# Kernel tuning notes

Measured on AMD Instinct MI355X. Metric: run time of the kernel, lower is better.

The kernel has to match this reference:

```python
import jax, jax.numpy as jnp
import numpy as np

PATCH = 16
EMBED = 384
BINS = 32
LN_EPS = 1e-5


def setup_inputs() -> dict:
    key = jax.random.key(0)
    k1, k2 = jax.random.split(key, 2)
    images = jax.random.uniform(k1, (64, 3, 224, 224), dtype=jnp.float32)  # pixels in [0,1]
    proj_w = jax.random.normal(k2, (EMBED, 3, PATCH, PATCH), dtype=jnp.float32) * 0.02  # OIHW
    proj_b = jnp.zeros((EMBED,), jnp.float32)
    ln_gamma = jnp.ones((EMBED,), jnp.float32)
    ln_beta = jnp.zeros((EMBED,), jnp.float32)
    return {"images": images, "proj_w": proj_w, "proj_b": proj_b,
            "ln_gamma": ln_gamma, "ln_beta": ln_beta}


def _patch_entropy(images, patch_size):
    # images: (B, C, H, W) in [0,1]
    B, C, H, W = images.shape
    gH, gW = H // patch_size, W // patch_size
    gray = images.mean(axis=1)  # (B, H, W)
    # non-overlapping patches -> (B, N, P*P)
    patches = gray.reshape(B, gH, patch_size, gW, patch_size)
    patches = patches.transpose(0, 1, 3, 2, 4).reshape(B, gH * gW, patch_size * patch_size)
    # quantize to 32 bins (floor, matching torch .long() on non-negative values)
    q = jnp.clip(patches * (BINS - 1), 0, BINS - 1).astype(jnp.int32)
    one_hot = jax.nn.one_hot(q, BINS, dtype=jnp.float32)      # (B, N, P*P, 32)
    hist = one_hot.sum(axis=2)                                 # (B, N, 32)
    prob = hist / jnp.maximum(hist.sum(axis=-1, keepdims=True), 1e-8)
    log_prob = jnp.log2(prob + 1e-10)
    entropy = -(prob * log_prob).sum(axis=-1)                  # (B, N)
    return entropy / np.float32(np.log2(BINS))


def reference(images, proj_w, proj_b, ln_gamma, ln_beta):
    p = PATCH
    B, C, H, W = images.shape
    gH, gW = H // p, W // p
    entropy = _patch_entropy(images, p)
    # patch-embed conv: kernel=stride=patch_size, VALID padding
    x = jax.lax.conv_general_dilated(
        images, proj_w, window_strides=(p, p), padding='VALID',
        dimension_numbers=('NCHW', 'OIHW', 'NCHW'))            # (B, D, gH, gW)
    x = x + proj_b[None, :, None, None]
    x = x.transpose(0, 2, 3, 1).reshape(B, gH * gW, -1)        # (B, N, D)
    mu = x.mean(axis=-1, keepdims=True)
    var = x.var(axis=-1, keepdims=True)                        # biased, like torch LayerNorm
    x = (x - mu) / jnp.sqrt(var + LN_EPS) * ln_gamma + ln_beta
    return x, entropy
```

## Files before the change

### kernel.cpp

```cpp
#include <hip/hip_runtime.h>

#define BATCH 64
#define GH 14
#define GW 14
#define NPATCH (GH*GW)
#define M_ROWS (BATCH*NPATCH)
#define KDIM 768
#define DDIM 384
#define HW (224*224)

typedef __attribute__((ext_vector_type(8))) short s16x8;
typedef __attribute__((ext_vector_type(4))) float f32x4;
typedef __attribute__((ext_vector_type(4))) unsigned short u16x4;

__device__ __forceinline__ unsigned short f2bf(float f) {
    unsigned int u = __float_as_uint(f);
    u += 0x7fff + ((u >> 16) & 1);
    return (unsigned short)(u >> 16);
}

__device__ __forceinline__ s16x8 cvt8(float4 lo, float4 hi) {
    s16x8 o;
    o[0] = (short)f2bf(lo.x); o[1] = (short)f2bf(lo.y);
    o[2] = (short)f2bf(lo.z); o[3] = (short)f2bf(lo.w);
    o[4] = (short)f2bf(hi.x); o[5] = (short)f2bf(hi.y);
    o[6] = (short)f2bf(hi.z); o[7] = (short)f2bf(hi.w);
    return o;
}

__global__ __launch_bounds__(256) void wcast_kernel(const float* __restrict__ w,
                                                    unsigned short* __restrict__ W) {
    int t = blockIdx.x * 256 + threadIdx.x;
    float4 v = ((const float4*)w)[t];
    u16x4 o = { f2bf(v.x), f2bf(v.y), f2bf(v.z), f2bf(v.w) };
    *(u16x4*)(W + t * 4) = o;
}

__global__ __launch_bounds__(384) void fused_kernel(const float* __restrict__ img,
                                                    const unsigned short* __restrict__ Bt,
                                                    const float* __restrict__ bias,
                                                    const float* __restrict__ gamma,
                                                    const float* __restrict__ beta,
                                                    float* __restrict__ C,
                                                    float* __restrict__ ent) {
    __shared__ __align__(16) unsigned short As[32 * 64];
    __shared__ __align__(16) unsigned short Bs[384 * 64];
    __shared__ int hist[6][32];
    __shared__ float sred[32], sred2[32], smean[32], srstd[32];

    const int tid  = threadIdx.x;
    const int lane = tid & 63;
    const int wv   = tid >> 6;
    const int quad = lane >> 4;
    const int cl   = lane & 15;
    const int rowBase = blockIdx.x * 32;

    if (tid < 32) { sred[tid] = 0.0f; sred2[tid] = 0.0f; }

    const int r1  = tid >> 3, ksg = tid & 7;
    const int sA1 = r1 * 64 + (ksg ^ (r1 & 7)) * 8;
    const float* pA1;
    {
        int p = rowBase + r1, b = p / NPATCH, n = p - b * NPATCH;
        int ph = n / GW, pw_ = n - ph * GW;
        pA1 = img + (size_t)b * (3 * HW) + (ph * 16 + (ksg >> 1)) * 224 + pw_ * 16 + (ksg & 1) * 8;
    }
    const unsigned short* pB0 = Bt + (size_t)(tid >> 3) * KDIM + (tid & 7) * 8;
    const int sB = (tid >> 3) * 64 + ((tid & 7) ^ ((tid >> 3) & 7)) * 8;

    s16x8 breg[8];
#pragma unroll
    for (int i = 0; i < 8; ++i)
        breg[i] = *(const s16x8*)(pB0 + (size_t)i * (48 * KDIM));
    float4 a1lo, a1hi;
    if (tid < 256) {
        a1lo = *(const float4*)(pA1);
        a1hi = *(const float4*)(pA1 + 4);
    }

    {
        const int pr  = lane >> 2;
        const int cc4 = (lane & 3) * 4;
        int p0 = rowBase + wv, b0 = p0 / NPATCH, n0i = p0 - b0 * NPATCH;
        int ph0 = n0i / GW, pw0 = n0i - ph0 * GW;
        const float* bp = img + (size_t)b0 * (3 * HW) + (ph0 * 16 + pr) * 224 + pw0 * 16 + cc4;
        float4 c0 = *(const float4*)(bp);
        float4 c1 = *(const float4*)(bp + HW);
        float4 c2 = *(const float4*)(bp + 2 * HW);
        for (int pp = wv; pp < 32; pp += 6) {
            float4 n0, n1, n2;
            if (pp + 6 < 32) {
                int p = rowBase + pp + 6, b = p / NPATCH, n = p - b * NPATCH;
                int ph = n / GW, pw_ = n - ph * GW;
                const float* np = img + (size_t)b * (3 * HW) + (ph * 16 + pr) * 224 + pw_ * 16 + cc4;
                n0 = *(const float4*)(np);
                n1 = *(const float4*)(np + HW);
                n2 = *(const float4*)(np + 2 * HW);
            }
            if (lane < 32) hist[wv][lane] = 0;
            asm volatile("s_waitcnt lgkmcnt(0)" ::: "memory");
            float g[4] = { (c0.x + c1.x + c2.x) / 3.0f, (c0.y + c1.y + c2.y) / 3.0f,
                           (c0.z + c1.z + c2.z) / 3.0f, (c0.w + c1.w + c2.w) / 3.0f };
#pragma unroll
            for (int j = 0; j < 4; ++j) {
                int bin = (int)(g[j] * 31.0f);
                bin = bin < 0 ? 0 : (bin > 31 ? 31 : bin);
                atomicAdd(&hist[wv][bin], 1);
            }
            asm volatile("s_waitcnt lgkmcnt(0)" ::: "memory");
            float t = 0.0f;
            if (lane < 32) {
                float prb = (float)hist[wv][lane] * (1.0f / 256.0f);
                t = -prb * log2f(prb + 1e-10f);
            }
#pragma unroll
            for (int off = 32; off; off >>= 1) t += __shfl_xor(t, off);
            if (lane == 0) ent[rowBase + pp] = t * (1.0f / 5.0f);
            c0 = n0; c1 = n1; c2 = n2;
        }
    }

    if (tid < 256) *(s16x8*)(As + sA1) = cvt8(a1lo, a1hi);
#pragma unroll
    for (int i = 0; i < 8; ++i)
        *(s16x8*)(Bs + sB + i * (48 * 64)) = breg[i];
    __syncthreads();

    f32x4 acc[2][4] = {};
    for (int kt = 0; kt < 12; ++kt) {
        if (kt < 11) {
            const int kn = kt + 1;
            if (tid < 256) {
                const float* pa = pA1 + (kn >> 2) * HW + (kn & 3) * (4 * 224);
                a1lo = *(const float4*)(pa);
                a1hi = *(const float4*)(pa + 4);
            }
#pragma unroll
            for (int i = 0; i < 8; ++i)
                breg[i] = *(const s16x8*)(pB0 + (size_t)i * (48 * KDIM) + kn * 64);
        }
#pragma unroll
        for (int ks = 0; ks < 2; ++ks) {
            const int sw = (ks * 4 + quad) ^ (cl & 7);
            s16x8 a_frag[2], b_frag[4];
#pragma unroll
            for (int i = 0; i < 2; ++i)
                a_frag[i] = *(const s16x8*)(As + (i * 16 + cl) * 64 + sw * 8);
#pragma unroll
            for (int j = 0; j < 4; ++j)
                b_frag[j] = *(const s16x8*)(Bs + (wv * 64 + j * 16 + cl) * 64 + sw * 8);
#pragma unroll
            for (int i = 0; i < 2; ++i)
#pragma unroll
                for (int j = 0; j < 4; ++j)
                    acc[i][j] = __builtin_amdgcn_mfma_f32_16x16x32_bf16(
                        a_frag[i], b_frag[j], acc[i][j], 0, 0, 0);
        }
        __syncthreads();
        if (kt < 11) {
            if (tid < 256) *(s16x8*)(As + sA1) = cvt8(a1lo, a1hi);
#pragma unroll
            for (int i = 0; i < 8; ++i)
                *(s16x8*)(Bs + sB + i * (48 * 64)) = breg[i];
        }
        __syncthreads();
    }

    float bv[4], gv[4], btv[4];
#pragma unroll
    for (int j = 0; j < 4; ++j) {
        int col = wv * 64 + j * 16 + cl;
        bv[j] = bias[col]; gv[j] = gamma[col]; btv[j] = beta[col];
    }

#pragma unroll
    for (int i = 0; i < 2; ++i) {
#pragma unroll
        for (int r = 0; r < 4; ++r) {
            float s1 = 0.0f, s2 = 0.0f;
#pragma unroll
            for (int j = 0; j < 4; ++j) {
                float v = acc[i][j][r] + bv[j];
                s1 += v; s2 += v * v;
            }
#pragma unroll
            for (int off = 1; off < 16; off <<= 1) {
                s1 += __shfl_xor(s1, off);
                s2 += __shfl_xor(s2, off);
            }
            if (cl == 0) {
                int row = i * 16 + quad * 4 + r;
                atomicAdd(&sred[row], s1);
                atomicAdd(&sred2[row], s2);
            }
        }
    }
    __syncthreads();
    if (tid < 32) {
        float mu  = sred[tid] * (1.0f / (float)DDIM);
        float var = sred2[tid] * (1.0f / (float)DDIM) - mu * mu;
        smean[tid] = mu;
        srstd[tid] = rsqrtf(var + 1e-5f);
    }
    __syncthreads();

#pragma unroll
    for (int i = 0; i < 2; ++i) {
#pragma unroll
        for (int r = 0; r < 4; ++r) {
            int row = i * 16 + quad * 4 + r;
            float mu = smean[row], rs = srstd[row];
            float* crow = C + (size_t)(rowBase + row) * DDIM;
#pragma unroll
            for (int j = 0; j < 4; ++j)
                crow[wv * 64 + j * 16 + cl] = (acc[i][j][r] + bv[j] - mu) * rs * gv[j] + btv[j];
        }
    }
}

extern "C" void kernel_launch(void* const* d_in, const int* in_sizes, int n_in,
                              void* d_out, int out_size, void* d_ws, size_t ws_size,
                              hipStream_t stream) {
    const float* img = (const float*)d_in[0];
    const float* pw  = (const float*)d_in[1];
    const float* pb  = (const float*)d_in[2];
    const float* gam = (const float*)d_in[3];
    const float* bet = (const float*)d_in[4];
    float* out = (float*)d_out;

    unsigned short* Wbf = (unsigned short*)d_ws;
    float* ent = out + (size_t)M_ROWS * DDIM;

    hipLaunchKernelGGL(wcast_kernel, dim3(288), dim3(256), 0, stream, pw, Wbf);
    hipLaunchKernelGGL(fused_kernel, dim3(392), dim3(384), 0, stream,
                       img, Wbf, pb, gam, bet, out, ent);
}
```

Baseline: 113.7 us.

## Load weight fragments directly into registers and double-buffer A tiles in LDS

Removes the shared-memory staging of the weight matrix: each wave now loads its MFMA B fragments straight from global memory into registers, with even/odd k-tile register sets prefetched one step ahead. The A tile is double-buffered across two LDS buffers with a register prefetch pipeline, which removes one barrier per k-step. LDS use drops sharply, and launch bounds request 3 blocks per CU for higher occupancy. The cost is more VGPR pressure and uncoalesced, redundant global reads of the weights across blocks, which now rely on the L2 cache.

```diff
diff --git a/kernel.cpp b/kernel.cpp
--- a/kernel.cpp
+++ b/kernel.cpp
@@ -36,15 +36,15 @@
     *(u16x4*)(W + t * 4) = o;
 }
 
-__global__ __launch_bounds__(384) void fused_kernel(const float* __restrict__ img,
-                                                    const unsigned short* __restrict__ Bt,
-                                                    const float* __restrict__ bias,
-                                                    const float* __restrict__ gamma,
-                                                    const float* __restrict__ beta,
-                                                    float* __restrict__ C,
-                                                    float* __restrict__ ent) {
-    __shared__ __align__(16) unsigned short As[32 * 64];
-    __shared__ __align__(16) unsigned short Bs[384 * 64];
+__global__ __launch_bounds__(384, 3) void fused_kernel(const float* __restrict__ img,
+                                                       const unsigned short* __restrict__ Bt,
+                                                       const float* __restrict__ bias,
+                                                       const float* __restrict__ gamma,
+                                                       const float* __restrict__ beta,
+                                                       float* __restrict__ C,
+                                                       float* __restrict__ ent) {
+    __shared__ __align__(16) unsigned short As0[32 * 64];
+    __shared__ __align__(16) unsigned short As1[32 * 64];
     __shared__ int hist[6][32];
     __shared__ float sred[32], sred2[32], smean[32], srstd[32];
 
@@ -65,17 +65,26 @@
         int ph = n / GW, pw_ = n - ph * GW;
         pA1 = img + (size_t)b * (3 * HW) + (ph * 16 + (ksg >> 1)) * 224 + pw_ * 16 + (ksg & 1) * 8;
     }
-    const unsigned short* pB0 = Bt + (size_t)(tid >> 3) * KDIM + (tid & 7) * 8;
-    const int sB = (tid >> 3) * 64 + ((tid & 7) ^ ((tid >> 3) & 7)) * 8;
-
-    s16x8 breg[8];
-#pragma unroll
-    for (int i = 0; i < 8; ++i)
-        breg[i] = *(const s16x8*)(pB0 + (size_t)i * (48 * KDIM));
-    float4 a1lo, a1hi;
+    const unsigned short* pBr = Bt + (size_t)(wv * 64 + cl) * KDIM + quad * 8;
+
+    s16x8 bE[8], bO[8];
+#pragma unroll
+    for (int j = 0; j < 4; ++j)
+#pragma unroll
+        for (int ks = 0; ks < 2; ++ks) {
+            bE[ks * 4 + j] = *(const s16x8*)(pBr + j * (16 * KDIM) + 0 * 64 + ks * 32);
+            bO[ks * 4 + j] = *(const s16x8*)(pBr + j * (16 * KDIM) + 1 * 64 + ks * 32);
+        }
+    float4 a0lo, a0hi, aOlo, aOhi, aElo, aEhi;
     if (tid < 256) {
-        a1lo = *(const float4*)(pA1);
-        a1hi = *(const float4*)(pA1 + 4);
+        a0lo = *(const float4*)(pA1);
+        a0hi = *(const float4*)(pA1 + 4);
+        const float* p1 = pA1 + 1 * (4 * 224);
+        aOlo = *(const float4*)(p1);
+        aOhi = *(const float4*)(p1 + 4);
+        const float* p2 = pA1 + 2 * (4 * 224);
+        aElo = *(const float4*)(p2);
+        aEhi = *(const float4*)(p2 + 4);
     }
 
     {
@@ -120,50 +129,65 @@
         }
     }
 
-    if (tid < 256) *(s16x8*)(As + sA1) = cvt8(a1lo, a1hi);
-#pragma unroll
-    for (int i = 0; i < 8; ++i)
-        *(s16x8*)(Bs + sB + i * (48 * 64)) = breg[i];
+    if (tid < 256) *(s16x8*)(As0 + sA1) = cvt8(a0lo, a0hi);
     __syncthreads();
 
     f32x4 acc[2][4] = {};
-    for (int kt = 0; kt < 12; ++kt) {
-        if (kt < 11) {
-            const int kn = kt + 1;
-            if (tid < 256) {
-                const float* pa = pA1 + (kn >> 2) * HW + (kn & 3) * (4 * 224);
-                a1lo = *(const float4*)(pa);
-                a1hi = *(const float4*)(pa + 4);
-            }
-#pragma unroll
-            for (int i = 0; i < 8; ++i)
-                breg[i] = *(const s16x8*)(pB0 + (size_t)i * (48 * KDIM) + kn * 64);
+#pragma unroll
+    for (int h = 0; h < 6; ++h) {
+        const int t0 = 2 * h;
+        if (tid < 256) *(s16x8*)(As1 + sA1) = cvt8(aOlo, aOhi);
+        if (h < 5 && tid < 256) {
+            const int kn = t0 + 3;
+            const float* p = pA1 + (kn >> 2) * HW + (kn & 3) * (4 * 224);
+            aOlo = *(const float4*)(p);
+            aOhi = *(const float4*)(p + 4);
         }
 #pragma unroll
         for (int ks = 0; ks < 2; ++ks) {
             const int sw = (ks * 4 + quad) ^ (cl & 7);
-            s16x8 a_frag[2], b_frag[4];
-#pragma unroll
-            for (int i = 0; i < 2; ++i)
-                a_frag[i] = *(const s16x8*)(As + (i * 16 + cl) * 64 + sw * 8);
+            s16x8 af0 = *(const s16x8*)(As0 + (0 * 16 + cl) * 64 + sw * 8);
+            s16x8 af1 = *(const s16x8*)(As0 + (1 * 16 + cl) * 64 + sw * 8);
+#pragma unroll
+            for (int j = 0; j < 4; ++j) {
+                acc[0][j] = __builtin_amdgcn_mfma_f32_16x16x32_bf16(af0, bE[ks * 4 + j], acc[0][j], 0, 0, 0);
+                acc[1][j] = __builtin_amdgcn_mfma_f32_16x16x32_bf16(af1, bE[ks * 4 + j], acc[1][j], 0, 0, 0);
+            }
+        }
+        if (h < 5) {
 #pragma unroll
             for (int j = 0; j < 4; ++j)
-                b_frag[j] = *(const s16x8*)(Bs + (wv * 64 + j * 16 + cl) * 64 + sw * 8);
-#pragma unroll
-            for (int i = 0; i < 2; ++i)
-#pragma unroll
-                for (int j = 0; j < 4; ++j)
-                    acc[i][j] = __builtin_amdgcn_mfma_f32_16x16x32_bf16(
-                        a_frag[i], b_frag[j], acc[i][j], 0, 0, 0);
+#pragma unroll
+                for (int ks = 0; ks < 2; ++ks)
+                    bE[ks * 4 + j] = *(const s16x8*)(pBr + j * (16 * KDIM) + (t0 + 2) * 64 + ks * 32);
         }
         __syncthreads();
-        if (kt < 11) {
-            if (tid < 256) *(s16x8*)(As + sA1) = cvt8(a1lo, a1hi);
-#pragma unroll
-            for (int i = 0; i < 8; ++i)
-                *(s16x8*)(Bs + sB + i * (48 * 64)) = breg[i];
-        }
-        __syncthreads();
+        if (h < 5 && tid < 256) *(s16x8*)(As0 + sA1) = cvt8(aElo, aEhi);
+        if (h < 4 && tid < 256) {
+            const int kn = t0 + 4;
+            const float* p = pA1 + (kn >> 2) * HW + (kn & 3) * (4 * 224);
+            aElo = *(const float4*)(p);
+            aEhi = *(const float4*)(p + 4);
+        }
+#pragma unroll
+        for (int ks = 0; ks < 2; ++ks) {
+            const int sw = (ks * 4 + quad) ^ (cl & 7);
+            s16x8 af0 = *(const s16x8*)(As1 + (0 * 16 + cl) * 64 + sw * 8);
+            s16x8 af1 = *(const s16x8*)(As1 + (1 * 16 + cl) * 64 + sw * 8);
+#pragma unroll
+            for (int j = 0; j < 4; ++j) {
+                acc[0][j] = __builtin_amdgcn_mfma_f32_16x16x32_bf16(af0, bO[ks * 4 + j], acc[0][j], 0, 0, 0);
+                acc[1][j] = __builtin_amdgcn_mfma_f32_16x16x32_bf16(af1, bO[ks * 4 + j], acc[1][j], 0, 0, 0);
+            }
+        }
+        if (h < 5) {
+#pragma unroll
+            for (int j = 0; j < 4; ++j)
+#pragma unroll
+                for (int ks = 0; ks < 2; ++ks)
+                    bO[ks * 4 + j] = *(const s16x8*)(pBr + j * (16 * KDIM) + (t0 + 3) * 64 + ks * 32);
+        }
+        if (h < 5) __syncthreads();
     }
 
     float bv[4], gv[4], btv[4];
```

Result: slower. 131.4 us (+15.6%).

## Load B fragments directly into registers and double-buffer A in shared memory

Applied to the files above, without the earlier changes.

Each wave now loads its weight (B) MFMA fragments straight from global memory into registers, so the B tile no longer goes through shared memory. The A tile moves to a two-buffer ping-pong, which cuts the synchronizations per k-step from two to one. Launch bounds now ask for two blocks per CU, which the much smaller LDS footprint allows. The trade-off is that the B register loads for the next step are issued right after the MFMAs with little latency hiding, and there is more register pressure.

```diff
diff --git a/kernel.cpp b/kernel.cpp
--- a/kernel.cpp
+++ b/kernel.cpp
@@ -36,15 +36,15 @@
     *(u16x4*)(W + t * 4) = o;
 }
 
-__global__ __launch_bounds__(384) void fused_kernel(const float* __restrict__ img,
-                                                    const unsigned short* __restrict__ Bt,
-                                                    const float* __restrict__ bias,
-                                                    const float* __restrict__ gamma,
-                                                    const float* __restrict__ beta,
-                                                    float* __restrict__ C,
-                                                    float* __restrict__ ent) {
-    __shared__ __align__(16) unsigned short As[32 * 64];
-    __shared__ __align__(16) unsigned short Bs[384 * 64];
+__global__ __launch_bounds__(384, 2) void fused_kernel(const float* __restrict__ img,
+                                                       const unsigned short* __restrict__ Bt,
+                                                       const float* __restrict__ bias,
+                                                       const float* __restrict__ gamma,
+                                                       const float* __restrict__ beta,
+                                                       float* __restrict__ C,
+                                                       float* __restrict__ ent) {
+    __shared__ __align__(16) unsigned short As0[32 * 64];
+    __shared__ __align__(16) unsigned short As1[32 * 64];
     __shared__ int hist[6][32];
     __shared__ float sred[32], sred2[32], smean[32], srstd[32];
 
@@ -65,17 +65,21 @@
         int ph = n / GW, pw_ = n - ph * GW;
         pA1 = img + (size_t)b * (3 * HW) + (ph * 16 + (ksg >> 1)) * 224 + pw_ * 16 + (ksg & 1) * 8;
     }
-    const unsigned short* pB0 = Bt + (size_t)(tid >> 3) * KDIM + (tid & 7) * 8;
-    const int sB = (tid >> 3) * 64 + ((tid & 7) ^ ((tid >> 3) & 7)) * 8;
-
-    s16x8 breg[8];
-#pragma unroll
-    for (int i = 0; i < 8; ++i)
-        breg[i] = *(const s16x8*)(pB0 + (size_t)i * (48 * KDIM));
-    float4 a1lo, a1hi;
+    const unsigned short* pBr = Bt + (size_t)(wv * 64 + cl) * KDIM + quad * 8;
+
+    s16x8 bcur[8];
+#pragma unroll
+    for (int j = 0; j < 4; ++j)
+#pragma unroll
+        for (int ks = 0; ks < 2; ++ks)
+            bcur[ks * 4 + j] = *(const s16x8*)(pBr + j * (16 * KDIM) + ks * 32);
+    float4 a0lo, a0hi, aNlo, aNhi;
     if (tid < 256) {
-        a1lo = *(const float4*)(pA1);
-        a1hi = *(const float4*)(pA1 + 4);
+        a0lo = *(const float4*)(pA1);
+        a0hi = *(const float4*)(pA1 + 4);
+        const float* p1 = pA1 + 1 * (4 * 224);
+        aNlo = *(const float4*)(p1);
+        aNhi = *(const float4*)(p1 + 4);
     }
 
     {
@@ -120,50 +124,41 @@
         }
     }
 
-    if (tid < 256) *(s16x8*)(As + sA1) = cvt8(a1lo, a1hi);
-#pragma unroll
-    for (int i = 0; i < 8; ++i)
-        *(s16x8*)(Bs + sB + i * (48 * 64)) = breg[i];
+    if (tid < 256) *(s16x8*)(As0 + sA1) = cvt8(a0lo, a0hi);
     __syncthreads();
 
     f32x4 acc[2][4] = {};
-    for (int kt = 0; kt < 12; ++kt) {
-        if (kt < 11) {
-            const int kn = kt + 1;
-            if (tid < 256) {
-                const float* pa = pA1 + (kn >> 2) * HW + (kn & 3) * (4 * 224);
-                a1lo = *(const float4*)(pa);
-                a1hi = *(const float4*)(pa + 4);
-            }
-#pragma unroll
-            for (int i = 0; i < 8; ++i)
-                breg[i] = *(const s16x8*)(pB0 + (size_t)i * (48 * KDIM) + kn * 64);
+#pragma unroll
+    for (int t = 0; t < 12; ++t) {
+        unsigned short* Aw = (t & 1) ? As0 : As1;
+        const unsigned short* Ar = (t & 1) ? As1 : As0;
+        if (t < 11 && tid < 256)
+            *(s16x8*)(Aw + sA1) = cvt8(aNlo, aNhi);
+        if (t < 10 && tid < 256) {
+            const int kn = t + 2;
+            const float* p = pA1 + (kn >> 2) * HW + (kn & 3) * (4 * 224);
+            aNlo = *(const float4*)(p);
+            aNhi = *(const float4*)(p + 4);
         }
 #pragma unroll
         for (int ks = 0; ks < 2; ++ks) {
             const int sw = (ks * 4 + quad) ^ (cl & 7);
-            s16x8 a_frag[2], b_frag[4];
-#pragma unroll
-            for (int i = 0; i < 2; ++i)
-                a_frag[i] = *(const s16x8*)(As + (i * 16 + cl) * 64 + sw * 8);
+            s16x8 af0 = *(const s16x8*)(Ar + (0 * 16 + cl) * 64 + sw * 8);
+            s16x8 af1 = *(const s16x8*)(Ar + (1 * 16 + cl) * 64 + sw * 8);
+#pragma unroll
+            for (int j = 0; j < 4; ++j) {
+                acc[0][j] = __builtin_amdgcn_mfma_f32_16x16x32_bf16(af0, bcur[ks * 4 + j], acc[0][j], 0, 0, 0);
+                acc[1][j] = __builtin_amdgcn_mfma_f32_16x16x32_bf16(af1, bcur[ks * 4 + j], acc[1][j], 0, 0, 0);
+            }
+        }
+        if (t < 11) {
 #pragma unroll
             for (int j = 0; j < 4; ++j)
-                b_frag[j] = *(const s16x8*)(Bs + (wv * 64 + j * 16 + cl) * 64 + sw * 8);
-#pragma unroll
-            for (int i = 0; i < 2; ++i)
-#pragma unroll
-                for (int j = 0; j < 4; ++j)
-                    acc[i][j] = __builtin_amdgcn_mfma_f32_16x16x32_bf16(
-                        a_frag[i], b_frag[j], acc[i][j], 0, 0, 0);
-        }
-        __syncthreads();
-        if (kt < 11) {
-            if (tid < 256) *(s16x8*)(As + sA1) = cvt8(a1lo, a1hi);
-#pragma unroll
-            for (int i = 0; i < 8; ++i)
-                *(s16x8*)(Bs + sB + i * (48 * 64)) = breg[i];
-        }
-        __syncthreads();
+#pragma unroll
+                for (int ks = 0; ks < 2; ++ks)
+                    bcur[ks * 4 + j] = *(const s16x8*)(pBr + j * (16 * KDIM) + (t + 1) * 64 + ks * 32);
+            __syncthreads();
+        }
     }
 
     float bv[4], gv[4], btv[4];
```

Result: slower. 125.7 us (+10.6%).
